# Kernel optimization log

Measured on AMD Instinct MI355X. Metric: run time of the kernel, lower is better.

The kernel has to match this reference:

```python
import jax, jax.numpy as jnp
import numpy as np

B, F, T, K = 4096, 2048, 16, 8


def setup_inputs() -> dict:
    key = jax.random.key(0)
    k1, k2, k3 = jax.random.split(key, 3)
    h_ens = jax.random.normal(k1, (B, F, T), dtype=jnp.float32)
    # Stacked per-(task, timestep) Linear(num_in_feat, 1) weights and biases.
    # nn.Linear default init ~ U(-1/sqrt(F), 1/sqrt(F)); plain normals are fine for a numeric reference.
    W = jax.random.normal(k2, (K, T, F), dtype=jnp.float32) * (1.0 / np.sqrt(F))
    b = jax.random.normal(k3, (K, T), dtype=jnp.float32) * (1.0 / np.sqrt(F))
    return {"h_ens": h_ens, "W": W, "b": b}


def reference(h_ens, W, b):
    # h_ens: [B, F, T], W: [K, T, F], b: [K, T]
    # logits[b, t, k] = sum_f h_ens[b, f, t] * W[k, t, f] + b[k, t]
    logits = jnp.einsum('bft,ktf->btk', h_ens, W) + b.T[None, :, :]
    return jax.nn.sigmoid(logits)  # [B, T, K]
```

## Files before the change

kernel.cpp:

```cpp
#include <hip/hip_runtime.h>
#include <math.h>

#define B_TOT 4096
#define F_DIM 2048
#define T_DIM 16
#define K_DIM 8
#define NB    4
#define SF    64
#define NSUP  (F_DIM / SF)

__device__ __forceinline__ void gload_lds16(const float* g, float* l) {
    __builtin_amdgcn_global_load_lds(
        (const __attribute__((address_space(1))) void*)g,
        (__attribute__((address_space(3))) void*)l,
        16, 0, 0);
}

__global__ __launch_bounds__(256)
void ta_kernel(const float* __restrict__ h, const float* __restrict__ W,
               const float* __restrict__ bias, float* __restrict__ out)
{
    __shared__ float smem[8192];

    const int tid = threadIdx.x;
    const int tp  = tid & 7;
    const int fr  = tid >> 3;
    const int b0  = blockIdx.x * NB;

    float acc[NB][2][K_DIM];
#pragma unroll
    for (int nb = 0; nb < NB; ++nb)
#pragma unroll
        for (int ts = 0; ts < 2; ++ts)
#pragma unroll
            for (int k = 0; k < K_DIM; ++k) acc[nb][ts][k] = 0.f;

    const int tl = tid >> 4;
    const int j4 = ((tid & 15) - tl) & 15;
    const float* wp = W + tl * F_DIM + j4 * 4;
    float* lp = smem + tid * 4;

    int voff[2][2];
#pragma unroll
    for (int il = 0; il < 2; ++il)
#pragma unroll
        for (int ts = 0; ts < 2; ++ts) {
            const int t = 2 * tp + ts;
            voff[il][ts] = t * 64 + ((il * 8 + (fr >> 2) + t) & 15) * 4 + (fr & 3);
        }

    const float2* hb = (const float2*)h + (size_t)b0 * 16384 + fr * 8 + tp;

    float2 hA[2][NB], hB[2][NB];

    auto loadh = [&](float2 (&buf)[2][NB], int sc) {
#pragma unroll
        for (int il = 0; il < 2; ++il)
#pragma unroll
            for (int nb = 0; nb < NB; ++nb)
                buf[il][nb] = hb[(size_t)nb * 16384 + sc * 512 + il * 256];
    };

    auto tile = [&](int sc, float2 (&cur)[2][NB], float2 (&nxt)[2][NB],
                    bool pf, int scn) {
        __syncthreads();
        {
            const float* wpf = wp + sc * SF;
#pragma unroll
            for (int r = 0; r < K_DIM; ++r)
                gload_lds16(wpf + r * (T_DIM * F_DIM), lp + r * 1024);
        }
        __syncthreads();
        if (pf) loadh(nxt, scn);

#pragma unroll
        for (int il = 0; il < 2; ++il)
#pragma unroll
            for (int ts = 0; ts < 2; ++ts) {
                float wv[K_DIM];
#pragma unroll
                for (int k = 0; k < K_DIM; ++k)
                    wv[k] = smem[k * 1024 + voff[il][ts]];
#pragma unroll
                for (int nb = 0; nb < NB; ++nb) {
                    const float hx = ts ? cur[il][nb].y : cur[il][nb].x;
#pragma unroll
                    for (int k = 0; k < K_DIM; ++k)
                        acc[nb][ts][k] = fmaf(hx, wv[k], acc[nb][ts][k]);
                }
            }
    };

    loadh(hA, 0);
    for (int sc = 0; sc < NSUP; sc += 2) {
        tile(sc,     hA, hB, true,          sc + 1);
        tile(sc + 1, hB, hA, sc + 2 < NSUP, sc + 2);
    }

#pragma unroll
    for (int c = 0; c < 2; ++c) {
        __syncthreads();
#pragma unroll
        for (int nbl = 0; nbl < 2; ++nbl)
#pragma unroll
            for (int ts = 0; ts < 2; ++ts) {
                const int t = 2 * tp + ts;
#pragma unroll
                for (int k = 0; k < K_DIM; ++k)
                    smem[(nbl * 16 + t) * 256 + k * 32 + ((fr + tp * 4) & 31)]
                        = acc[c * 2 + nbl][ts][k];
            }
        __syncthreads();
        const int nbl = tid >> 7, rem = tid & 127, tt = rem >> 3, kk = rem & 7;
        float s = 0.f;
#pragma unroll
        for (int j = 0; j < 32; ++j)
            s += smem[(nbl * 16 + tt) * 256 + kk * 32 + ((tid + j) & 31)];
        s += bias[kk * T_DIM + tt];
        s = 1.0f / (1.0f + __expf(-s));
        out[(size_t)(b0 + c * 2 + nbl) * (T_DIM * K_DIM) + rem] = s;
    }
}

extern "C" void kernel_launch(void* const* d_in, const int* in_sizes, int n_in,
                              void* d_out, int out_size, void* d_ws, size_t ws_size,
                              hipStream_t stream) {
    const float* h    = (const float*)d_in[0];
    const float* W    = (const float*)d_in[1];
    const float* bias = (const float*)d_in[2];
    float* out = (float*)d_out;
    ta_kernel<<<dim3(B_TOT / NB), dim3(256), 0, stream>>>(h, W, bias, out);
}
```

Before: 697.0 us.

## Load W directly into registers instead of staging through LDS

Removes the per-tile global_load_lds staging of W and the two barriers per tile, and has each thread load its own W float2 values straight from global memory into registers. It double-buffers both h and W in registers across supertiles. The f-to-thread mapping changes so each thread handles two adjacent f values per load. This drops synchronization and LDS traffic, but adds redundant global/L2 reads of W across threads and blocks and raises register pressure.

```diff
diff --git a/kernel.cpp b/kernel.cpp
--- a/kernel.cpp
+++ b/kernel.cpp
@@ -9,12 +9,6 @@
 #define SF    64
 #define NSUP  (F_DIM / SF)
 
-__device__ __forceinline__ void gload_lds16(const float* g, float* l) {
-    __builtin_amdgcn_global_load_lds(
-        (const __attribute__((address_space(1))) void*)g,
-        (__attribute__((address_space(3))) void*)l,
-        16, 0, 0);
-}
 
 __global__ __launch_bounds__(256)
 void ta_kernel(const float* __restrict__ h, const float* __restrict__ W,
@@ -24,7 +18,7 @@
 
     const int tid = threadIdx.x;
     const int tp  = tid & 7;
-    const int fr  = tid >> 3;
+    const int fp  = tid >> 3;
     const int b0  = blockIdx.x * NB;
 
     float acc[NB][2][K_DIM];
@@ -35,66 +29,54 @@
 #pragma unroll
             for (int k = 0; k < K_DIM; ++k) acc[nb][ts][k] = 0.f;
 
-    const int tl = tid >> 4;
-    const int j4 = ((tid & 15) - tl) & 15;
-    const float* wp = W + tl * F_DIM + j4 * 4;
-    float* lp = smem + tid * 4;
+    const float2* h2 = (const float2*)h;
+    unsigned ho[NB];
+#pragma unroll
+    for (int nb = 0; nb < NB; ++nb)
+        ho[nb] = (unsigned)(b0 + nb) * 16384u + (unsigned)(fp * 16 + tp);
 
-    int voff[2][2];
+    unsigned wo[2];
 #pragma unroll
-    for (int il = 0; il < 2; ++il)
+    for (int ts = 0; ts < 2; ++ts)
+        wo[ts] = (unsigned)((2 * tp + ts) * 2048 + 2 * fp);
+
+    float2 hA[2 * NB], hB[2 * NB];
+    float2 wA[2 * K_DIM], wB[2 * K_DIM];
+
+    auto LH = [&](float2 (&buf)[2 * NB], int sc) {
 #pragma unroll
-        for (int ts = 0; ts < 2; ++ts) {
-            const int t = 2 * tp + ts;
-            voff[il][ts] = t * 64 + ((il * 8 + (fr >> 2) + t) & 15) * 4 + (fr & 3);
-        }
-
-    const float2* hb = (const float2*)h + (size_t)b0 * 16384 + fr * 8 + tp;
-
-    float2 hA[2][NB], hB[2][NB];
-
-    auto loadh = [&](float2 (&buf)[2][NB], int sc) {
+        for (int nb = 0; nb < NB; ++nb)
 #pragma unroll
-        for (int il = 0; il < 2; ++il)
+            for (int d = 0; d < 2; ++d)
+                buf[nb * 2 + d] = h2[ho[nb] + (unsigned)(sc * 512 + d * 8)];
+    };
+    auto LW = [&](float2 (&buf)[2 * K_DIM], int sc) {
 #pragma unroll
-            for (int nb = 0; nb < NB; ++nb)
-                buf[il][nb] = hb[(size_t)nb * 16384 + sc * 512 + il * 256];
+        for (int k = 0; k < K_DIM; ++k)
+#pragma unroll
+            for (int ts = 0; ts < 2; ++ts)
+                buf[k * 2 + ts] = *(const float2*)(W + k * 32768 + (int)wo[ts] + sc * 64);
+    };
+    auto DO_FMA = [&](float2 (&hv)[2 * NB], float2 (&wv)[2 * K_DIM]) {
+#pragma unroll
+        for (int k = 0; k < K_DIM; ++k)
+#pragma unroll
+            for (int ts = 0; ts < 2; ++ts)
+#pragma unroll
+                for (int nb = 0; nb < NB; ++nb) {
+                    const float h0 = ts ? hv[nb * 2 + 0].y : hv[nb * 2 + 0].x;
+                    const float h1 = ts ? hv[nb * 2 + 1].y : hv[nb * 2 + 1].x;
+                    acc[nb][ts][k] = fmaf(h0, wv[k * 2 + ts].x, acc[nb][ts][k]);
+                    acc[nb][ts][k] = fmaf(h1, wv[k * 2 + ts].y, acc[nb][ts][k]);
+                }
     };
 
-    auto tile = [&](int sc, float2 (&cur)[2][NB], float2 (&nxt)[2][NB],
-                    bool pf, int scn) {
-        __syncthreads();
-        {
-            const float* wpf = wp + sc * SF;
-#pragma unroll
-            for (int r = 0; r < K_DIM; ++r)
-                gload_lds16(wpf + r * (T_DIM * F_DIM), lp + r * 1024);
-        }
-        __syncthreads();
-        if (pf) loadh(nxt, scn);
-
-#pragma unroll
-        for (int il = 0; il < 2; ++il)
-#pragma unroll
-            for (int ts = 0; ts < 2; ++ts) {
-                float wv[K_DIM];
-#pragma unroll
-                for (int k = 0; k < K_DIM; ++k)
-                    wv[k] = smem[k * 1024 + voff[il][ts]];
-#pragma unroll
-                for (int nb = 0; nb < NB; ++nb) {
-                    const float hx = ts ? cur[il][nb].y : cur[il][nb].x;
-#pragma unroll
-                    for (int k = 0; k < K_DIM; ++k)
-                        acc[nb][ts][k] = fmaf(hx, wv[k], acc[nb][ts][k]);
-                }
-            }
-    };
-
-    loadh(hA, 0);
+    LH(hA, 0); LW(wA, 0);
     for (int sc = 0; sc < NSUP; sc += 2) {
-        tile(sc,     hA, hB, true,          sc + 1);
-        tile(sc + 1, hB, hA, sc + 2 < NSUP, sc + 2);
+        LH(hB, sc + 1); LW(wB, sc + 1);
+        DO_FMA(hA, wA);
+        if (sc + 2 < NSUP) { LH(hA, sc + 2); LW(wA, sc + 2); }
+        DO_FMA(hB, wB);
     }
 
 #pragma unroll
@@ -107,7 +89,7 @@
                 const int t = 2 * tp + ts;
 #pragma unroll
                 for (int k = 0; k < K_DIM; ++k)
-                    smem[(nbl * 16 + t) * 256 + k * 32 + ((fr + tp * 4) & 31)]
+                    smem[(nbl * 16 + t) * 256 + k * 32 + ((fp + tp * 4) & 31)]
                         = acc[c * 2 + nbl][ts][k];
             }
         __syncthreads();
```

New measurement: 798.8 us. 1.15x slower.

## Give each wavefront private double-buffered weight slices and drop per-tile block barriers

Applied to the files above, without the earlier changes.

Each wavefront now stages its own slice of W into a private double-buffered LDS region, so the two __syncthreads per tile are replaced by s_waitcnt vmcnt counting plus sched_barrier. The next tile's h loads and W global-to-LDS copies are issued before computing on the current tile, overlapping memory with FMAs. LDS use doubles to 64KB, which may reduce occupancy. Correctness relies on the vmcnt(16) count exactly matching the outstanding loads and on each wave reading only its own staged data.

```diff
diff --git a/kernel.cpp b/kernel.cpp
--- a/kernel.cpp
+++ b/kernel.cpp
@@ -16,16 +16,22 @@
         16, 0, 0);
 }
 
+
 __global__ __launch_bounds__(256)
 void ta_kernel(const float* __restrict__ h, const float* __restrict__ W,
                const float* __restrict__ bias, float* __restrict__ out)
 {
-    __shared__ float smem[8192];
+    __shared__ float smem[16384];
 
-    const int tid = threadIdx.x;
-    const int tp  = tid & 7;
-    const int fr  = tid >> 3;
-    const int b0  = blockIdx.x * NB;
+    const int tid  = threadIdx.x;
+    const int lane = tid & 63;
+    const int wid  = tid >> 6;
+    const int tp   = tid & 7;
+    const int frl  = (tid >> 3) & 7;
+    const int b0   = blockIdx.x * NB;
+
+    float* const wbuf0 = smem + wid * 4096;
+    float* const wbuf1 = wbuf0 + 2048;
 
     float acc[NB][2][K_DIM];
 #pragma unroll
@@ -35,44 +41,37 @@
 #pragma unroll
             for (int k = 0; k < K_DIM; ++k) acc[nb][ts][k] = 0.f;
 
-    const int tl = tid >> 4;
-    const int j4 = ((tid & 15) - tl) & 15;
-    const float* wp = W + tl * F_DIM + j4 * 4;
-    float* lp = smem + tid * 4;
+    const int tl  = (lane & 7) * 2 + (lane >> 5);
+    const int flb = ((lane >> 3) & 3) * 4;
+    const float* const wsrc = W + tl * F_DIM + wid * 16 + flb;
+    float* const ldst0 = wbuf0 + lane * 4;
+    float* const ldst1 = wbuf1 + lane * 4;
 
-    int voff[2][2];
+    int rdo[2][2];
 #pragma unroll
     for (int il = 0; il < 2; ++il)
 #pragma unroll
-        for (int ts = 0; ts < 2; ++ts) {
-            const int t = 2 * tp + ts;
-            voff[il][ts] = t * 64 + ((il * 8 + (fr >> 2) + t) & 15) * 4 + (fr & 3);
-        }
+        for (int ts = 0; ts < 2; ++ts)
+            rdo[il][ts] = ts * 128 + (il * 2 + (frl >> 2)) * 32 + tp * 4 + (frl & 3);
 
-    const float2* hb = (const float2*)h + (size_t)b0 * 16384 + fr * 8 + tp;
+    const float2* const hb =
+        (const float2*)h + (size_t)b0 * 16384 + wid * 128 + frl * 8 + tp;
 
-    float2 hA[2][NB], hB[2][NB];
+    float2 hA[2 * NB], hB[2 * NB];
 
-    auto loadh = [&](float2 (&buf)[2][NB], int sc) {
+    auto LH = [&](float2 (&buf)[2 * NB], int sc) {
 #pragma unroll
-        for (int il = 0; il < 2; ++il)
+        for (int nb = 0; nb < NB; ++nb)
 #pragma unroll
-            for (int nb = 0; nb < NB; ++nb)
-                buf[il][nb] = hb[(size_t)nb * 16384 + sc * 512 + il * 256];
+            for (int il = 0; il < 2; ++il)
+                buf[nb * 2 + il] = hb[nb * 16384 + sc * 512 + il * 64];
     };
-
-    auto tile = [&](int sc, float2 (&cur)[2][NB], float2 (&nxt)[2][NB],
-                    bool pf, int scn) {
-        __syncthreads();
-        {
-            const float* wpf = wp + sc * SF;
+    auto STAGE = [&](float* ldst, int sc) {
 #pragma unroll
-            for (int r = 0; r < K_DIM; ++r)
-                gload_lds16(wpf + r * (T_DIM * F_DIM), lp + r * 1024);
-        }
-        __syncthreads();
-        if (pf) loadh(nxt, scn);
-
+        for (int k = 0; k < K_DIM; ++k)
+            gload_lds16(wsrc + k * (T_DIM * F_DIM) + sc * SF, ldst + k * 256);
+    };
+    auto COMP = [&](const float* sm, float2 (&hv)[2 * NB]) {
 #pragma unroll
         for (int il = 0; il < 2; ++il)
 #pragma unroll
@@ -80,10 +79,10 @@
                 float wv[K_DIM];
 #pragma unroll
                 for (int k = 0; k < K_DIM; ++k)
-                    wv[k] = smem[k * 1024 + voff[il][ts]];
+                    wv[k] = sm[k * 256 + rdo[il][ts]];
 #pragma unroll
                 for (int nb = 0; nb < NB; ++nb) {
-                    const float hx = ts ? cur[il][nb].y : cur[il][nb].x;
+                    const float hx = ts ? hv[nb * 2 + il].y : hv[nb * 2 + il].x;
 #pragma unroll
                     for (int k = 0; k < K_DIM; ++k)
                         acc[nb][ts][k] = fmaf(hx, wv[k], acc[nb][ts][k]);
@@ -91,12 +90,30 @@
             }
     };
 
-    loadh(hA, 0);
-    for (int sc = 0; sc < NSUP; sc += 2) {
-        tile(sc,     hA, hB, true,          sc + 1);
-        tile(sc + 1, hB, hA, sc + 2 < NSUP, sc + 2);
+    LH(hA, 0);
+    STAGE(ldst0, 0);
+
+#define ITERX(sc, LDNXT, HCUR, HNXT, SMCUR)                        \
+    do {                                                           \
+        LH(HNXT, (sc) + 1);                                        \
+        STAGE(LDNXT, (sc) + 1);                                    \
+        asm volatile("s_waitcnt vmcnt(16)" ::: "memory");          \
+        __builtin_amdgcn_sched_barrier(0);                         \
+        COMP(SMCUR, HCUR);                                         \
+    } while (0)
+
+#pragma unroll 1
+    for (int p = 0; p < 15; ++p) {
+        ITERX(2 * p,     ldst1, hA, hB, wbuf0);
+        ITERX(2 * p + 1, ldst0, hB, hA, wbuf1);
     }
+    ITERX(30, ldst1, hA, hB, wbuf0);
+    asm volatile("s_waitcnt vmcnt(0)" ::: "memory");
+    __builtin_amdgcn_sched_barrier(0);
+    COMP(wbuf1, hB);
+#undef ITERX
 
+    const int fp = tid >> 3;
 #pragma unroll
     for (int c = 0; c < 2; ++c) {
         __syncthreads();
@@ -107,7 +124,7 @@
                 const int t = 2 * tp + ts;
 #pragma unroll
                 for (int k = 0; k < K_DIM; ++k)
-                    smem[(nbl * 16 + t) * 256 + k * 32 + ((fr + tp * 4) & 31)]
+                    smem[(nbl * 16 + t) * 256 + k * 32 + ((fp + tp * 4) & 31)]
                         = acc[c * 2 + nbl][ts][k];
             }
         __syncthreads();
```

Measured after the change: 732.8 us. 5.1% more time.
